# Kernel tuning notes

Measured on AMD Instinct MI355X. Metric: run time of the kernel, lower is better.

## Reference

```python
import jax, jax.numpy as jnp
import numpy as np
import math

B, S, D = 4, 2048, 1024
H, DH = 16, 64  # num_heads, head dim (hardcoded 64 in module)


def setup_inputs() -> dict:
    key = jax.random.key(0)
    ks = jax.random.split(key, 5)
    scale = 0.02
    return {
        "x": jax.random.normal(ks[0], (B, S, D), dtype=jnp.float32),
        "W_Q": jax.random.normal(ks[1], (D, H * DH), dtype=jnp.float32) * scale,
        "W_K": jax.random.normal(ks[2], (D, H * DH), dtype=jnp.float32) * scale,
        "W_V": jax.random.normal(ks[3], (D, H * DH), dtype=jnp.float32) * scale,
        "W_O": jax.random.normal(ks[4], (H * DH, D), dtype=jnp.float32) * scale,
        "ln_gamma": jnp.ones((D,), dtype=jnp.float32),
        "ln_beta": jnp.zeros((D,), dtype=jnp.float32),
    }


def reference(x, W_Q, W_K, W_V, W_O, ln_gamma, ln_beta):
    # QKV projections (bias=False Linear: x @ W)
    q = (x @ W_Q).reshape(B, S, H, DH).transpose(0, 2, 1, 3)  # [B,H,S,DH]
    k = (x @ W_K).reshape(B, S, H, DH).transpose(0, 2, 1, 3)
    v = (x @ W_V).reshape(B, S, H, DH).transpose(0, 2, 1, 3)

    # scaled scores with causal mask (upper triangle, diag=1 -> -1e7)
    scores = jnp.einsum("bhsd,bhtd->bhst", q, k) / math.sqrt(DH)  # [B,H,S,S]
    causal = jnp.triu(jnp.ones((S, S), dtype=bool), k=1)
    scores = jnp.where(causal, jnp.float32(-1e7), scores)
    attn = jax.nn.softmax(scores, axis=-1)
    ctx = jnp.einsum("bhst,bhtd->bhsd", attn, v)  # [B,H,S,DH]

    # merge heads, output proj, residual, LayerNorm
    out = ctx.transpose(0, 2, 1, 3).reshape(B, S, H * DH) @ W_O + x
    mu = jnp.mean(out, axis=-1, keepdims=True)
    var = jnp.mean((out - mu) ** 2, axis=-1, keepdims=True)
    out = (out - mu) * jax.lax.rsqrt(var + 1e-5) * ln_gamma + ln_beta
    return out
```

## Files before the change

### kernel.cpp

```cpp
#include <hip/hip_runtime.h>
#include <hip/hip_bf16.h>
#include <cstdint>
#include <cstddef>

#define S_ 2048
#define D_ 1024
#define H_ 16
#define DH_ 64
#define M_ 8192

using bf16 = __bf16;
using bf16x4 = __attribute__((ext_vector_type(4))) __bf16;
using bf16x8 = __attribute__((ext_vector_type(8))) __bf16;
using f32x4 = __attribute__((ext_vector_type(4))) float;
using s16x4 = __attribute__((ext_vector_type(4))) short;

__device__ __forceinline__ void g2lds16(const bf16* g, bf16* l) {
  __builtin_amdgcn_global_load_lds(
      (const __attribute__((address_space(1))) void*)g,
      (__attribute__((address_space(3))) void*)l, 16, 0, 0);
}

__device__ __forceinline__ f32x4 mfma16(bf16x4 a, bf16x4 b, f32x4 c) {
#if __has_builtin(__builtin_amdgcn_mfma_f32_16x16x16_bf16)
  return __builtin_amdgcn_mfma_f32_16x16x16_bf16(a, b, c, 0, 0, 0);
#elif __has_builtin(__builtin_amdgcn_mfma_f32_16x16x16bf16_1k)
  return __builtin_amdgcn_mfma_f32_16x16x16bf16_1k(
      __builtin_bit_cast(s16x4, a), __builtin_bit_cast(s16x4, b), c, 0, 0, 0);
#else
  f32x4 d;
  asm("v_mfma_f32_16x16x16_bf16 %0, %1, %2, %3"
      : "=v"(d)
      : "v"(a), "v"(b), "v"(c));
  return d;
#endif
}

__global__ __launch_bounds__(256) void cvt_all_kernel(
    const float* __restrict__ x, const float* __restrict__ w0,
    const float* __restrict__ w1, const float* __restrict__ w2,
    const float* __restrict__ w3, bf16* __restrict__ xb,
    bf16* __restrict__ o0, bf16* __restrict__ o1, bf16* __restrict__ o2,
    bf16* __restrict__ o3) {
  __shared__ float tile[32][33];
  int bx = blockIdx.x;
  int tid = threadIdx.x;
  if (bx < 4096) {
    size_t i = ((size_t)bx * 256 + tid) * 8;
    float4 a = *(const float4*)(x + i);
    float4 b = *(const float4*)(x + i + 4);
    bf16x8 o;
    o[0] = (bf16)a.x; o[1] = (bf16)a.y; o[2] = (bf16)a.z; o[3] = (bf16)a.w;
    o[4] = (bf16)b.x; o[5] = (bf16)b.y; o[6] = (bf16)b.z; o[7] = (bf16)b.w;
    *(bf16x8*)(xb + i) = o;
    return;
  }
  int wb = bx - 4096;
  int wsel = wb >> 10; wb &= 1023;
  const float* W; bf16* O;
  switch (wsel) {
    case 0: W = w0; O = o0; break;
    case 1: W = w1; O = o1; break;
    case 2: W = w2; O = o2; break;
    default: W = w3; O = o3; break;
  }
  int n0 = (wb & 31) * 32;
  int k0 = (wb >> 5) * 32;
#pragma unroll
  for (int i = 0; i < 4; ++i) {
    int e = tid + i * 256; int rr = e >> 5, cc = e & 31;
    tile[rr][cc] = W[(size_t)(k0 + rr) * 1024 + n0 + cc];
  }
  __syncthreads();
#pragma unroll
  for (int i = 0; i < 4; ++i) {
    int e = tid + i * 256; int rr = e >> 5, cc = e & 31;
    O[(size_t)(n0 + rr) * 1024 + k0 + cc] = (bf16)tile[cc][rr];
  }
}

template <int MODE>
__global__ __launch_bounds__(256) void gemm_kernel(
    const bf16* __restrict__ A,
    const bf16* __restrict__ Bt0, const bf16* __restrict__ Bt1,
    const bf16* __restrict__ Bt2,
    bf16* __restrict__ Qo, bf16* __restrict__ Ko, bf16* __restrict__ Vto,
    const float* __restrict__ xres, float* __restrict__ out) {
  __shared__ __align__(16) bf16 smA0[128 * 32], smA1[128 * 32];
  __shared__ __align__(16) bf16 smB0[128 * 32], smB1[128 * 32];
  constexpr int NBLK = (MODE == 0) ? 24 : 8;
  int bm = blockIdx.x / NBLK, bn = blockIdx.x % NBLK;
  int m0 = bm * 128;
  const bf16* Bt; int which = 0, n0;
  if constexpr (MODE == 0) {
    which = bn >> 3; n0 = (bn & 7) * 128;
    Bt = (which == 0) ? Bt0 : (which == 1 ? Bt1 : Bt2);
  } else { n0 = bn * 128; Bt = Bt0; }

  int tid = threadIdx.x;
  int wave = tid >> 6, lane = tid & 63;
  int quad = lane >> 4, r = lane & 15;
  int wm = (wave >> 1) * 64, wn = (wave & 1) * 64;

  f32x4 acc[4][4];
  f32x4 zero = {0.f, 0.f, 0.f, 0.f};
#pragma unroll
  for (int i = 0; i < 4; ++i)
#pragma unroll
    for (int j = 0; j < 4; ++j) acc[i][j] = zero;

  int c0 = 2 * wave, c1 = 2 * wave + 1;
  int rA0 = c0 * 16 + (lane >> 2);
  int rA1 = c1 * 16 + (lane >> 2);
  int kc = ((lane & 3) ^ ((lane >> 3) & 3)) * 8;
  const int rx = (r >> 1) & 3;

  const bf16 *pA0, *pA1;
  if constexpr (MODE == 0) {
    pA0 = A + (size_t)(m0 + rA0) * 1024 + kc;
    pA1 = A + (size_t)(m0 + rA1) * 1024 + kc;
  } else {
    int mm0 = m0 + rA0, mm1 = m0 + rA1;
    pA0 = A + ((size_t)((mm0 >> 11) * H_) * S_ + (mm0 & 2047)) * DH_ + kc;
    pA1 = A + ((size_t)((mm1 >> 11) * H_) * S_ + (mm1 & 2047)) * DH_ + kc;
  }
  const bf16* pB0 = Bt + (size_t)(n0 + rA0) * 1024 + kc;
  const bf16* pB1 = Bt + (size_t)(n0 + rA1) * 1024 + kc;
  constexpr ptrdiff_t dEven = 32;
  constexpr ptrdiff_t dOdd = (MODE == 0) ? 32 : (ptrdiff_t)S_ * DH_ - 32;

  bf16* dstA0 = smA0 + c0 * 512; bf16* dstA0b = smA0 + c1 * 512;
  bf16* dstA1 = smA1 + c0 * 512; bf16* dstA1b = smA1 + c1 * 512;
  bf16* dstB0 = smB0 + c0 * 512; bf16* dstB0b = smB0 + c1 * 512;
  bf16* dstB1 = smB1 + c0 * 512; bf16* dstB1b = smB1 + c1 * 512;

  g2lds16(pA0, dstA0); g2lds16(pA1, dstA0b);
  g2lds16(pB0, dstB0); g2lds16(pB1, dstB0b);
  pA0 += dEven; pA1 += dEven; pB0 += dEven; pB1 += dEven;

  const int roA = (wm + r) * 32 + (quad ^ rx) * 8;
  const int roB = (wn + r) * 32 + (quad ^ rx) * 8;

  auto compute = [&](const bf16* bufA, const bf16* bufB) {
    bf16x8 af[4], bfr[4];
#pragma unroll
    for (int i = 0; i < 4; ++i) af[i] = *(const bf16x8*)(bufA + roA + i * 512);
#pragma unroll
    for (int j = 0; j < 4; ++j) bfr[j] = *(const bf16x8*)(bufB + roB + j * 512);
    if (which == 2) {
#pragma unroll
      for (int i = 0; i < 4; ++i)
#pragma unroll
        for (int j = 0; j < 4; ++j)
          acc[i][j] = __builtin_amdgcn_mfma_f32_16x16x32_bf16(bfr[i], af[j],
                                                              acc[i][j], 0, 0, 0);
    } else {
#pragma unroll
      for (int i = 0; i < 4; ++i)
#pragma unroll
        for (int j = 0; j < 4; ++j)
          acc[i][j] = __builtin_amdgcn_mfma_f32_16x16x32_bf16(af[i], bfr[j],
                                                              acc[i][j], 0, 0, 0);
    }
  };

#pragma unroll 1
  for (int kt = 0; kt < 32; kt += 2) {
    g2lds16(pA0, dstA1); g2lds16(pA1, dstA1b);
    g2lds16(pB0, dstB1); g2lds16(pB1, dstB1b);
    pA0 += dOdd; pA1 += dOdd; pB0 += dEven; pB1 += dEven;
    asm volatile("s_waitcnt vmcnt(4)\n\ts_barrier" ::: "memory");
    compute(smA0, smB0);
    asm volatile("s_waitcnt lgkmcnt(0)\n\ts_barrier" ::: "memory");
    if (kt + 2 < 32) {
      g2lds16(pA0, dstA0); g2lds16(pA1, dstA0b);
      g2lds16(pB0, dstB0); g2lds16(pB1, dstB0b);
      pA0 += dEven; pA1 += dEven; pB0 += dEven; pB1 += dEven;
      asm volatile("s_waitcnt vmcnt(4)\n\ts_barrier" ::: "memory");
    } else {
      asm volatile("s_waitcnt vmcnt(0)\n\ts_barrier" ::: "memory");
    }
    compute(smA1, smB1);
    asm volatile("s_waitcnt lgkmcnt(0)\n\ts_barrier" ::: "memory");
  }

  if (which == 2) {
#pragma unroll
    for (int i = 0; i < 4; ++i) {
#pragma unroll
      for (int j = 0; j < 4; ++j) {
#pragma unroll
        for (int g = 0; g < 4; ++g) {
          int n = n0 + wn + i * 16 + quad * 4 + g;
          int m = m0 + wm + j * 16 + r;
          Vto[((size_t)((m >> 11) * H_ + (n >> 6)) * DH_ + (n & 63)) * S_ +
              (m & 2047)] = (bf16)acc[i][j][g];
        }
      }
    }
    return;
  }
#pragma unroll
  for (int i = 0; i < 4; ++i) {
#pragma unroll
    for (int j = 0; j < 4; ++j) {
#pragma unroll
      for (int g = 0; g < 4; ++g) {
        int m = m0 + wm + i * 16 + quad * 4 + g;
        int n = n0 + wn + j * 16 + r;
        float v = acc[i][j][g];
        if constexpr (MODE == 0) {
          int b = m >> 11, s = m & 2047, h = n >> 6, dh = n & 63;
          if (which == 0)
            Qo[((size_t)(b * H_ + h) * S_ + s) * DH_ + dh] = (bf16)v;
          else
            Ko[((size_t)(b * H_ + h) * S_ + s) * DH_ + dh] = (bf16)v;
        } else {
          size_t idx = (size_t)m * 1024 + n;
          out[idx] = v + xres[idx];
        }
      }
    }
  }
}

__global__ __launch_bounds__(256) void attn_kernel(const bf16* __restrict__ Qb,
                                                   const bf16* __restrict__ Kb,
                                                   const bf16* __restrict__ Vtb,
                                                   bf16* __restrict__ ctx) {
  __shared__ __align__(16) bf16 smK[2][64 * 64];
  __shared__ __align__(16) bf16 smV[2][64 * 64];
  const int bh = blockIdx.x & 63, p = blockIdx.x >> 6;
  const bf16* Qh = Qb + (size_t)bh * S_ * DH_;
  const bf16* Kh = Kb + (size_t)bh * S_ * DH_;
  const bf16* Vh = Vtb + (size_t)bh * DH_ * S_;
  bf16* Ch = ctx + (size_t)bh * S_ * DH_;
  const int tid = threadIdx.x, wave = tid >> 6, lane = tid & 63;
  const int quad = lane >> 4, r = lane & 15;
  const int r7 = r & 7;
  const int c0 = 2 * wave, c1 = c0 + 1;
  const int sr = lane >> 3;
  const int gcol = ((lane & 7) ^ (sr & 7)) * 8;
  const f32x4 zero = {0.f, 0.f, 0.f, 0.f};
  const int xk0 = (quad ^ r7) * 8, xk1 = ((quad + 4) ^ r7) * 8;

  for (int ph = 0; ph < 2; ++ph) {
    const int i128 = ph ? (15 - p) : p;
    const int qB = i128 * 128;
    const int q0w = qB + wave * 32;
    const int numkt = 2 * i128 + 2;

    bf16x8 qf[2][2];
    const float qsc = 0.125f * 1.44269504f;
#pragma unroll
    for (int qg = 0; qg < 2; ++qg)
#pragma unroll
      for (int hh = 0; hh < 2; ++hh) {
        bf16x8 q = *(const bf16x8*)(Qh + (size_t)(q0w + qg * 16 + r) * DH_ +
                                    hh * 32 + quad * 8);
#pragma unroll
        for (int i = 0; i < 8; ++i) q[i] = (bf16)((float)q[i] * qsc);
        qf[qg][hh] = q;
      }

    f32x4 lacc[2] = {zero, zero};
    f32x4 oacc[2][4];
#pragma unroll
    for (int qg = 0; qg < 2; ++qg)
#pragma unroll
      for (int tn = 0; tn < 4; ++tn) oacc[qg][tn] = zero;

    g2lds16(Kh + (size_t)(c0 * 8 + sr) * DH_ + gcol, &smK[0][c0 * 512]);
    g2lds16(Kh + (size_t)(c1 * 8 + sr) * DH_ + gcol, &smK[0][c1 * 512]);
    g2lds16(Vh + (size_t)(c0 * 8 + sr) * S_ + gcol, &smV[0][c0 * 512]);
    g2lds16(Vh + (size_t)(c1 * 8 + sr) * S_ + gcol, &smV[0][c1 * 512]);

    for (int kt = 0; kt < numkt; ++kt) {
      const int cur = kt & 1;
      const int kv0 = kt * 64;
      if (kt + 1 < numkt) {
        const int nk = kv0 + 64;
        g2lds16(Kh + (size_t)(nk + c0 * 8 + sr) * DH_ + gcol, &smK[1 - cur][c0 * 512]);
        g2lds16(Kh + (size_t)(nk + c1 * 8 + sr) * DH_ + gcol, &smK[1 - cur][c1 * 512]);
        g2lds16(Vh + (size_t)(c0 * 8 + sr) * S_ + nk + gcol, &smV[1 - cur][c0 * 512]);
        g2lds16(Vh + (size_t)(c1 * 8 + sr) * S_ + nk + gcol, &smV[1 - cur][c1 * 512]);
        asm volatile("s_waitcnt vmcnt(4)\n\ts_barrier" ::: "memory");
      } else {
        asm volatile("s_waitcnt vmcnt(0)\n\ts_barrier" ::: "memory");
      }
      if (kv0 <= q0w + 31) {
        const bf16* kb = &smK[cur][0];
        const bf16* vb = &smV[cur][0];

        f32x4 s[2][4];
#pragma unroll
        for (int t = 0; t < 4; ++t) {
          bf16x8 kf0 = *(const bf16x8*)(kb + (t * 16 + r) * 64 + xk0);
          bf16x8 kf1 = *(const bf16x8*)(kb + (t * 16 + r) * 64 + xk1);
#pragma unroll
          for (int qg = 0; qg < 2; ++qg) {
            f32x4 z = __builtin_amdgcn_mfma_f32_16x16x32_bf16(kf0, qf[qg][0],
                                                              zero, 0, 0, 0);
            s[qg][t] = __builtin_amdgcn_mfma_f32_16x16x32_bf16(kf1, qf[qg][1],
                                                               z, 0, 0, 0);
          }
        }
        if (kt >= numkt - 2) {
#pragma unroll
          for (int qg = 0; qg < 2; ++qg) {
            const int q = q0w + qg * 16 + r;
#pragma unroll
            for (int t = 0; t < 4; ++t) {
              const int kv = kv0 + t * 16 + quad * 4;
#pragma unroll
              for (int g = 0; g < 4; ++g)
                if (kv + g > q) s[qg][t][g] = -1e30f;
            }
          }
        }
#pragma unroll
        for (int t = 0; t < 4; ++t) {
          bf16x4 pa[2];
#pragma unroll
          for (int qg = 0; qg < 2; ++qg) {
#pragma unroll
            for (int g = 0; g < 4; ++g)
              s[qg][t][g] = __builtin_amdgcn_exp2f(s[qg][t][g]);
            lacc[qg] += s[qg][t];
            bf16x4 pk;
#pragma unroll
            for (int g = 0; g < 4; ++g) pk[g] = (bf16)s[qg][t][g];
            pa[qg] = pk;
          }
#pragma unroll
          for (int tn = 0; tn < 4; ++tn) {
            bf16x4 vf = *(const bf16x4*)(
                vb + (tn * 16 + r) * 64 +
                ((2 * t + (quad >> 1)) ^ r7) * 8 + (quad & 1) * 4);
            oacc[0][tn] = mfma16(pa[0], vf, oacc[0][tn]);
            oacc[1][tn] = mfma16(pa[1], vf, oacc[1][tn]);
          }
        }
      }
      asm volatile("s_waitcnt lgkmcnt(0)\n\ts_barrier" ::: "memory");
    }

#pragma unroll
    for (int qg = 0; qg < 2; ++qg) {
      float rs = (lacc[qg][0] + lacc[qg][1]) + (lacc[qg][2] + lacc[qg][3]);
      rs += __shfl_xor(rs, 16, 64);
      rs += __shfl_xor(rs, 32, 64);
      const float inv = 1.f / rs;
      f32x4 ib;
#pragma unroll
      for (int g = 0; g < 4; ++g) ib[g] = __shfl(inv, quad * 4 + g, 64);
#pragma unroll
      for (int tn = 0; tn < 4; ++tn) {
        f32x4 ov = oacc[qg][tn] * ib;
#pragma unroll
        for (int g = 0; g < 4; ++g)
          Ch[(size_t)(q0w + qg * 16 + quad * 4 + g) * DH_ + tn * 16 + r] =
              (bf16)ov[g];
      }
    }
  }
}

__global__ __launch_bounds__(256) void ln_kernel(float* __restrict__ out,
                                                 const float* __restrict__ gamma,
                                                 const float* __restrict__ beta) {
  __shared__ float red[8];
  size_t row = blockIdx.x;
  float* p = out + row * 1024;
  int tid = threadIdx.x;
  float4 v = ((const float4*)p)[tid];
  float s1 = v.x + v.y + v.z + v.w;
  float s2 = v.x * v.x + v.y * v.y + v.z * v.z + v.w * v.w;
#pragma unroll
  for (int o = 1; o < 64; o <<= 1) {
    s1 += __shfl_xor(s1, o, 64);
    s2 += __shfl_xor(s2, o, 64);
  }
  int wave = tid >> 6, lane = tid & 63;
  if (lane == 0) { red[wave] = s1; red[4 + wave] = s2; }
  __syncthreads();
  s1 = red[0] + red[1] + red[2] + red[3];
  s2 = red[4] + red[5] + red[6] + red[7];
  float mean = s1 * (1.f / 1024.f);
  float var = s2 * (1.f / 1024.f) - mean * mean;
  float rstd = rsqrtf(var + 1e-5f);
  float4 g = ((const float4*)gamma)[tid];
  float4 b = ((const float4*)beta)[tid];
  float4 o;
  o.x = (v.x - mean) * rstd * g.x + b.x;
  o.y = (v.y - mean) * rstd * g.y + b.y;
  o.z = (v.z - mean) * rstd * g.z + b.z;
  o.w = (v.w - mean) * rstd * g.w + b.w;
  ((float4*)p)[tid] = o;
}

extern "C" void kernel_launch(void* const* d_in, const int* in_sizes, int n_in,
                              void* d_out, int out_size, void* d_ws,
                              size_t ws_size, hipStream_t stream) {
  (void)in_sizes; (void)n_in; (void)out_size; (void)ws_size;
  const float* x  = (const float*)d_in[0];
  const float* WQ = (const float*)d_in[1];
  const float* WK = (const float*)d_in[2];
  const float* WV = (const float*)d_in[3];
  const float* WO = (const float*)d_in[4];
  const float* gamma = (const float*)d_in[5];
  const float* beta  = (const float*)d_in[6];
  float* out = (float*)d_out;

  bf16* ws = (bf16*)d_ws;
  const size_t MD = (size_t)M_ * D_;
  const size_t WW = (size_t)D_ * D_;
  bf16* xb   = ws;
  bf16* wqt  = xb + MD;
  bf16* wkt  = wqt + WW;
  bf16* wvt  = wkt + WW;
  bf16* wot  = wvt + WW;
  bf16* Qb   = wot + WW;
  bf16* Kb   = Qb + MD;
  bf16* Vtb  = Kb + MD;
  bf16* ctxb = Vtb + MD;

  cvt_all_kernel<<<dim3(8192), dim3(256), 0, stream>>>(
      x, WQ, WK, WV, WO, xb, wqt, wkt, wvt, wot);
  gemm_kernel<0><<<dim3(64 * 24), dim3(256), 0, stream>>>(
      xb, wqt, wkt, wvt, Qb, Kb, Vtb, nullptr, nullptr);
  attn_kernel<<<dim3(512), dim3(256), 0, stream>>>(Qb, Kb, Vtb, ctxb);
  gemm_kernel<1><<<dim3(64 * 8), dim3(256), 0, stream>>>(
      ctxb, wot, nullptr, nullptr, nullptr, nullptr, nullptr, x, out);
  ln_kernel<<<dim3(8192), dim3(256), 0, stream>>>(out, gamma, beta);
}
```

Before: 265.2 us.

## Restructure GEMM to 128x256 tiles with triple-buffered K=64 LDS pipeline

Rewrites the projection GEMMs to use 512-thread workgroups with 128x256 output tiles, K-steps of 64, and a three-stage async global-to-LDS pipeline in dynamic shared memory. It adds an XCD-aware block remap, raises MFMA issue priority with s_setprio, and writes V transposed through packed bf16x4 stores. The aim is more data reuse per LDS load, better latency hiding and better L2 locality. In exchange it uses 144KB of LDS per block and launches fewer, larger workgroups, which lowers occupancy and wave-level parallelism.

```diff
diff --git a/kernel.cpp b/kernel.cpp
--- a/kernel.cpp
+++ b/kernel.cpp
@@ -80,144 +80,187 @@
 }
 
 template <int MODE>
-__global__ __launch_bounds__(256) void gemm_kernel(
+__global__ __launch_bounds__(512, 2) void gemm_kernel(
     const bf16* __restrict__ A,
     const bf16* __restrict__ Bt0, const bf16* __restrict__ Bt1,
     const bf16* __restrict__ Bt2,
     bf16* __restrict__ Qo, bf16* __restrict__ Ko, bf16* __restrict__ Vto,
     const float* __restrict__ xres, float* __restrict__ out) {
-  __shared__ __align__(16) bf16 smA0[128 * 32], smA1[128 * 32];
-  __shared__ __align__(16) bf16 smB0[128 * 32], smB1[128 * 32];
-  constexpr int NBLK = (MODE == 0) ? 24 : 8;
-  int bm = blockIdx.x / NBLK, bn = blockIdx.x % NBLK;
-  int m0 = bm * 128;
-  const bf16* Bt; int which = 0, n0;
+  extern __shared__ float4 smem4[];
+  bf16* smem = (bf16*)smem4;
+
+  constexpr int NWG = (MODE == 0) ? 768 : 256;
+  constexpr int CPX = NWG / 8;
+  constexpr int NBN = (MODE == 0) ? 12 : 4;
+  const int wg = ((int)blockIdx.x & 7) * CPX + ((int)blockIdx.x >> 3);
+  const int bn = wg % NBN, bm = wg / NBN;
+
+  const bf16* Bt;
+  int n0full = 0, wsel = 0;
   if constexpr (MODE == 0) {
-    which = bn >> 3; n0 = (bn & 7) * 128;
-    Bt = (which == 0) ? Bt0 : (which == 1 ? Bt1 : Bt2);
-  } else { n0 = bn * 128; Bt = Bt0; }
-
-  int tid = threadIdx.x;
-  int wave = tid >> 6, lane = tid & 63;
-  int quad = lane >> 4, r = lane & 15;
-  int wm = (wave >> 1) * 64, wn = (wave & 1) * 64;
+    wsel = bn >> 2;
+    Bt = (wsel == 0) ? Bt0 : (wsel == 1 ? Bt1 : Bt2);
+    n0full = (bn & 3) * 256;
+  } else {
+    Bt = Bt0;
+    n0full = bn * 256;
+  }
+
+  const int tid = threadIdx.x;
+  const int wave = tid >> 6, lane = tid & 63;
+  const int quad = lane >> 4, r = lane & 15;
+  const int wm = (wave >> 2) * 64, wn = (wave & 3) * 64;
+
+  const int lrow = lane >> 3;
+  const int lcol = ((lane & 7) ^ lrow) * 8;
+  const int am0 = bm * 128 + wave * 8 + lrow;
+  const int am1 = am0 + 64;
+  const bf16 *p0, *p1, *p2, *p3, *p4, *p5;
+  if constexpr (MODE == 0) {
+    p0 = A + (size_t)am0 * 1024 + lcol;
+    p1 = A + (size_t)am1 * 1024 + lcol;
+  } else {
+    p0 = A + (size_t)(am0 >> 11) * (16 * (size_t)S_ * DH_) +
+         (size_t)(am0 & 2047) * 64 + lcol;
+    p1 = A + (size_t)(am1 >> 11) * (16 * (size_t)S_ * DH_) +
+         (size_t)(am1 & 2047) * 64 + lcol;
+  }
+  const int bnr = n0full + wave * 8 + lrow;
+  p2 = Bt + (size_t)bnr * 1024 + lcol;
+  p3 = Bt + (size_t)(bnr + 64) * 1024 + lcol;
+  p4 = Bt + (size_t)(bnr + 128) * 1024 + lcol;
+  p5 = Bt + (size_t)(bnr + 192) * 1024 + lcol;
+  constexpr ptrdiff_t dA = (MODE == 0) ? 64 : (ptrdiff_t)S_ * DH_;
+
+  const int oA0 = wave * 512, oA1 = (8 + wave) * 512;
+  const int oB0 = 8192 + wave * 512, oB1 = 8192 + (8 + wave) * 512;
+  const int oB2 = 8192 + (16 + wave) * 512, oB3 = 8192 + (24 + wave) * 512;
+
+  auto stage = [&](bf16* base) {
+    g2lds16(p0, base + oA0); p0 += dA;
+    g2lds16(p1, base + oA1); p1 += dA;
+    g2lds16(p2, base + oB0); p2 += 64;
+    g2lds16(p3, base + oB1); p3 += 64;
+    g2lds16(p4, base + oB2); p4 += 64;
+    g2lds16(p5, base + oB3); p5 += 64;
+  };
 
   f32x4 acc[4][4];
-  f32x4 zero = {0.f, 0.f, 0.f, 0.f};
+  const f32x4 zero = {0.f, 0.f, 0.f, 0.f};
 #pragma unroll
   for (int i = 0; i < 4; ++i)
 #pragma unroll
     for (int j = 0; j < 4; ++j) acc[i][j] = zero;
 
-  int c0 = 2 * wave, c1 = 2 * wave + 1;
-  int rA0 = c0 * 16 + (lane >> 2);
-  int rA1 = c1 * 16 + (lane >> 2);
-  int kc = ((lane & 3) ^ ((lane >> 3) & 3)) * 8;
-  const int rx = (r >> 1) & 3;
-
-  const bf16 *pA0, *pA1;
+  const int rw = r & 7;
+  const int x0 = (quad ^ rw) * 8;
+  const int x1 = ((quad + 4) ^ rw) * 8;
+  const int raB = (wm + r) * 64;
+  const int rbB = (wn + r) * 64;
+
+  auto phases = [&](const bf16* buf) {
+    const bf16* bA = buf;
+    const bf16* bB = buf + 8192;
+    bf16x8 af[4], bg[4];
+#pragma unroll
+    for (int i = 0; i < 4; ++i)
+      af[i] = *(const bf16x8*)(bA + raB + i * 1024 + x0);
+#pragma unroll
+    for (int j = 0; j < 4; ++j)
+      bg[j] = *(const bf16x8*)(bB + rbB + j * 1024 + x0);
+    __builtin_amdgcn_s_setprio(1);
+#pragma unroll
+    for (int i = 0; i < 4; ++i)
+#pragma unroll
+      for (int j = 0; j < 4; ++j)
+        acc[i][j] = __builtin_amdgcn_mfma_f32_16x16x32_bf16(af[i], bg[j],
+                                                            acc[i][j], 0, 0, 0);
+    __builtin_amdgcn_s_setprio(0);
+    asm volatile("s_barrier" ::: "memory");
+#pragma unroll
+    for (int i = 0; i < 4; ++i)
+      af[i] = *(const bf16x8*)(bA + raB + i * 1024 + x1);
+#pragma unroll
+    for (int j = 0; j < 4; ++j)
+      bg[j] = *(const bf16x8*)(bB + rbB + j * 1024 + x1);
+    __builtin_amdgcn_s_setprio(1);
+#pragma unroll
+    for (int i = 0; i < 4; ++i)
+#pragma unroll
+      for (int j = 0; j < 4; ++j)
+        acc[i][j] = __builtin_amdgcn_mfma_f32_16x16x32_bf16(af[i], bg[j],
+                                                            acc[i][j], 0, 0, 0);
+    __builtin_amdgcn_s_setprio(0);
+  };
+
+  bf16* b0 = smem;
+  bf16* b1 = smem + 24576;
+  bf16* b2 = smem + 49152;
+
+  stage(b0);
+  stage(b1);
+
+#pragma unroll 1
+  for (int kt = 0; kt < 15; kt += 3) {
+    asm volatile("s_waitcnt vmcnt(6)\n\ts_barrier" ::: "memory");
+    stage(b2);
+    phases(b0);
+    asm volatile("s_waitcnt vmcnt(6)\n\ts_barrier" ::: "memory");
+    stage(b0);
+    phases(b1);
+    asm volatile("s_waitcnt vmcnt(6)\n\ts_barrier" ::: "memory");
+    if (kt < 12) stage(b1);
+    phases(b2);
+  }
+  asm volatile("s_waitcnt vmcnt(0)\n\ts_barrier" ::: "memory");
+  phases(b0);
+
+  const int mB = bm * 128 + wm + quad * 4;
   if constexpr (MODE == 0) {
-    pA0 = A + (size_t)(m0 + rA0) * 1024 + kc;
-    pA1 = A + (size_t)(m0 + rA1) * 1024 + kc;
+    if (wsel < 2) {
+      bf16* dst = (wsel == 0) ? Qo : Ko;
+#pragma unroll
+      for (int i = 0; i < 4; ++i) {
+#pragma unroll
+        for (int j = 0; j < 4; ++j) {
+          int n = n0full + wn + j * 16 + r;
+          int h = n >> 6, dh = n & 63;
+#pragma unroll
+          for (int g = 0; g < 4; ++g) {
+            int m = mB + i * 16 + g;
+            int b = m >> 11, s = m & 2047;
+            dst[((size_t)(b * H_ + h) * S_ + s) * DH_ + dh] =
+                (bf16)acc[i][j][g];
+          }
+        }
+      }
+    } else {
+#pragma unroll
+      for (int i = 0; i < 4; ++i) {
+        int m = mB + i * 16;
+        int b = m >> 11, s = m & 2047;
+#pragma unroll
+        for (int j = 0; j < 4; ++j) {
+          int n = n0full + wn + j * 16 + r;
+          int h = n >> 6, dh = n & 63;
+          bf16x4 pk;
+#pragma unroll
+          for (int g = 0; g < 4; ++g) pk[g] = (bf16)acc[i][j][g];
+          *(bf16x4*)(Vto + ((size_t)(b * H_ + h) * DH_ + dh) * S_ + s) = pk;
+        }
+      }
+    }
   } else {
-    int mm0 = m0 + rA0, mm1 = m0 + rA1;
-    pA0 = A + ((size_t)((mm0 >> 11) * H_) * S_ + (mm0 & 2047)) * DH_ + kc;
-    pA1 = A + ((size_t)((mm1 >> 11) * H_) * S_ + (mm1 & 2047)) * DH_ + kc;
-  }
-  const bf16* pB0 = Bt + (size_t)(n0 + rA0) * 1024 + kc;
-  const bf16* pB1 = Bt + (size_t)(n0 + rA1) * 1024 + kc;
-  constexpr ptrdiff_t dEven = 32;
-  constexpr ptrdiff_t dOdd = (MODE == 0) ? 32 : (ptrdiff_t)S_ * DH_ - 32;
-
-  bf16* dstA0 = smA0 + c0 * 512; bf16* dstA0b = smA0 + c1 * 512;
-  bf16* dstA1 = smA1 + c0 * 512; bf16* dstA1b = smA1 + c1 * 512;
-  bf16* dstB0 = smB0 + c0 * 512; bf16* dstB0b = smB0 + c1 * 512;
-  bf16* dstB1 = smB1 + c0 * 512; bf16* dstB1b = smB1 + c1 * 512;
-
-  g2lds16(pA0, dstA0); g2lds16(pA1, dstA0b);
-  g2lds16(pB0, dstB0); g2lds16(pB1, dstB0b);
-  pA0 += dEven; pA1 += dEven; pB0 += dEven; pB1 += dEven;
-
-  const int roA = (wm + r) * 32 + (quad ^ rx) * 8;
-  const int roB = (wn + r) * 32 + (quad ^ rx) * 8;
-
-  auto compute = [&](const bf16* bufA, const bf16* bufB) {
-    bf16x8 af[4], bfr[4];
-#pragma unroll
-    for (int i = 0; i < 4; ++i) af[i] = *(const bf16x8*)(bufA + roA + i * 512);
-#pragma unroll
-    for (int j = 0; j < 4; ++j) bfr[j] = *(const bf16x8*)(bufB + roB + j * 512);
-    if (which == 2) {
-#pragma unroll
-      for (int i = 0; i < 4; ++i)
-#pragma unroll
-        for (int j = 0; j < 4; ++j)
-          acc[i][j] = __builtin_amdgcn_mfma_f32_16x16x32_bf16(bfr[i], af[j],
-                                                              acc[i][j], 0, 0, 0);
-    } else {
-#pragma unroll
-      for (int i = 0; i < 4; ++i)
-#pragma unroll
-        for (int j = 0; j < 4; ++j)
-          acc[i][j] = __builtin_amdgcn_mfma_f32_16x16x32_bf16(af[i], bfr[j],
-                                                              acc[i][j], 0, 0, 0);
-    }
-  };
-
-#pragma unroll 1
-  for (int kt = 0; kt < 32; kt += 2) {
-    g2lds16(pA0, dstA1); g2lds16(pA1, dstA1b);
-    g2lds16(pB0, dstB1); g2lds16(pB1, dstB1b);
-    pA0 += dOdd; pA1 += dOdd; pB0 += dEven; pB1 += dEven;
-    asm volatile("s_waitcnt vmcnt(4)\n\ts_barrier" ::: "memory");
-    compute(smA0, smB0);
-    asm volatile("s_waitcnt lgkmcnt(0)\n\ts_barrier" ::: "memory");
-    if (kt + 2 < 32) {
-      g2lds16(pA0, dstA0); g2lds16(pA1, dstA0b);
-      g2lds16(pB0, dstB0); g2lds16(pB1, dstB0b);
-      pA0 += dEven; pA1 += dEven; pB0 += dEven; pB1 += dEven;
-      asm volatile("s_waitcnt vmcnt(4)\n\ts_barrier" ::: "memory");
-    } else {
-      asm volatile("s_waitcnt vmcnt(0)\n\ts_barrier" ::: "memory");
-    }
-    compute(smA1, smB1);
-    asm volatile("s_waitcnt lgkmcnt(0)\n\ts_barrier" ::: "memory");
-  }
-
-  if (which == 2) {
 #pragma unroll
     for (int i = 0; i < 4; ++i) {
 #pragma unroll
       for (int j = 0; j < 4; ++j) {
+        int n = bn * 256 + wn + j * 16 + r;
 #pragma unroll
         for (int g = 0; g < 4; ++g) {
-          int n = n0 + wn + i * 16 + quad * 4 + g;
-          int m = m0 + wm + j * 16 + r;
-          Vto[((size_t)((m >> 11) * H_ + (n >> 6)) * DH_ + (n & 63)) * S_ +
-              (m & 2047)] = (bf16)acc[i][j][g];
-        }
-      }
-    }
-    return;
-  }
-#pragma unroll
-  for (int i = 0; i < 4; ++i) {
-#pragma unroll
-    for (int j = 0; j < 4; ++j) {
-#pragma unroll
-      for (int g = 0; g < 4; ++g) {
-        int m = m0 + wm + i * 16 + quad * 4 + g;
-        int n = n0 + wn + j * 16 + r;
-        float v = acc[i][j][g];
-        if constexpr (MODE == 0) {
-          int b = m >> 11, s = m & 2047, h = n >> 6, dh = n & 63;
-          if (which == 0)
-            Qo[((size_t)(b * H_ + h) * S_ + s) * DH_ + dh] = (bf16)v;
-          else
-            Ko[((size_t)(b * H_ + h) * S_ + s) * DH_ + dh] = (bf16)v;
-        } else {
+          int m = mB + i * 16 + g;
           size_t idx = (size_t)m * 1024 + n;
-          out[idx] = v + xres[idx];
+          out[idx] = acc[i][j][g] + xres[idx];
         }
       }
     }
@@ -425,12 +468,24 @@
   bf16* Vtb  = Kb + MD;
   bf16* ctxb = Vtb + MD;
 
+  constexpr int GEMM_LDS = 3 * 48 * 1024;
+  static bool s_attr = false;
+  if (!s_attr) {
+    s_attr = true;
+    (void)hipFuncSetAttribute(reinterpret_cast<const void*>(gemm_kernel<0>),
+                              hipFuncAttributeMaxDynamicSharedMemorySize,
+                              GEMM_LDS);
+    (void)hipFuncSetAttribute(reinterpret_cast<const void*>(gemm_kernel<1>),
+                              hipFuncAttributeMaxDynamicSharedMemorySize,
+                              GEMM_LDS);
+  }
+
   cvt_all_kernel<<<dim3(8192), dim3(256), 0, stream>>>(
       x, WQ, WK, WV, WO, xb, wqt, wkt, wvt, wot);
-  gemm_kernel<0><<<dim3(64 * 24), dim3(256), 0, stream>>>(
+  gemm_kernel<0><<<dim3(768), dim3(512), GEMM_LDS, stream>>>(
       xb, wqt, wkt, wvt, Qb, Kb, Vtb, nullptr, nullptr);
   attn_kernel<<<dim3(512), dim3(256), 0, stream>>>(Qb, Kb, Vtb, ctxb);
-  gemm_kernel<1><<<dim3(64 * 8), dim3(256), 0, stream>>>(
+  gemm_kernel<1><<<dim3(256), dim3(512), GEMM_LDS, stream>>>(
       ctxb, wot, nullptr, nullptr, nullptr, nullptr, nullptr, x, out);
   ln_kernel<<<dim3(8192), dim3(256), 0, stream>>>(out, gamma, beta);
 }
```

New measurement: 253.2 us. 4.5% less time.
